# Kernel tuning notes

Measured on AMD Instinct MI355X. Metric: run time of the kernel, lower is better.

Reference implementation:

```python
import jax, jax.numpy as jnp
import numpy as np

B, S, H, DH = 2, 2048, 16, 64
D = H * DH


def setup_inputs() -> dict:
    key = jax.random.key(0)
    ks = jax.random.split(key, 10)
    std = 0.02
    return {
        "hidden_states": jax.random.normal(ks[0], (B, S, D), jnp.float32),
        "mask": jax.random.randint(ks[1], (B, S), 0, 2, jnp.int64 if jax.config.jax_enable_x64 else jnp.int32),
        "Wq": jax.random.normal(ks[2], (D, D), jnp.float32) * std,
        "bq": jnp.zeros((D,), jnp.float32),
        "Wk": jax.random.normal(ks[3], (D, D), jnp.float32) * std,
        "bk": jnp.zeros((D,), jnp.float32),
        "Wv": jax.random.normal(ks[4], (D, D), jnp.float32) * std,
        "bv": jnp.zeros((D,), jnp.float32),
        "Wo": jax.random.normal(ks[5], (D, D), jnp.float32) * std,
        "bo": jnp.zeros((D,), jnp.float32),
    }


def _split_heads(x):
    # (B, S, H*DH) -> (B, H, S, DH)
    b, s, _ = x.shape
    return x.reshape(b, s, H, DH).transpose(0, 2, 1, 3)


def reference(hidden_states, mask, Wq, bq, Wk, bk, Wv, bv, Wo, bo):
    # Linear projections (torch nn.Linear: x @ W.T + b)
    q = _split_heads(hidden_states @ Wq.T + bq)
    k = _split_heads(hidden_states @ Wk.T + bk)
    v = _split_heads(hidden_states @ Wv.T + bv)

    scale = 1.0 / np.sqrt(DH).astype(np.float32)
    scores = jnp.einsum("bhqd,bhkd->bhqk", q, k) * scale  # (B,H,S,S)
    # mask out padded key positions (mask==0 -> -inf), broadcast over heads/queries
    scores = jnp.where(mask[:, None, None, :] == 0, -jnp.inf, scores)
    weights = jax.nn.softmax(scores, axis=-1)

    attended = jnp.einsum("bhqk,bhkd->bhqd", weights, v)  # (B,H,S,DH)
    merged = attended.transpose(0, 2, 1, 3).reshape(hidden_states.shape)  # (B,S,D)
    return merged @ Wo.T + bo
```

## Files before the change

kernel.cpp:

```cpp
#include <hip/hip_runtime.h>
#include <hip/hip_bf16.h>

typedef __bf16 bf16;
typedef __bf16 bf16x4 __attribute__((ext_vector_type(4)));
typedef __bf16 bf16x8 __attribute__((ext_vector_type(8)));
typedef float f32x4 __attribute__((ext_vector_type(4)));

#define B_ 2
#define S_ 2048
#define H_ 16
#define DH_ 64
#define D_ 1024
#define NT_ 4096

#define WAIT_VMCNT0() asm volatile("s_waitcnt vmcnt(0)" ::: "memory")
#define WAIT_LGKM0()  asm volatile("s_waitcnt lgkmcnt(0)" ::: "memory")

__device__ __forceinline__ void gld_lds16(const bf16* g, bf16* l) {
    __builtin_amdgcn_global_load_lds(
        (__attribute__((address_space(1))) void*)g,
        (__attribute__((address_space(3))) void*)l, 16, 0, 0);
}

__device__ __forceinline__ bf16 f2bf(float x) {
    union { float f; unsigned u; } v; v.f = x;
    unsigned short h = (unsigned short)((v.u + 0x7FFF + ((v.u >> 16) & 1)) >> 16);
    return __builtin_bit_cast(bf16, h);
}

__global__ __launch_bounds__(256) void cvt_kernel(
    const float* __restrict__ hs,
    const float* __restrict__ Wq, const float* __restrict__ Wk,
    const float* __restrict__ Wv, const float* __restrict__ Wo,
    bf16* __restrict__ hsb, bf16* __restrict__ wqkv, bf16* __restrict__ wob)
{
    int i = (blockIdx.x * 256 + threadIdx.x) * 4;
    const float* src;
    bf16* dst;
    if (i < 4194304) {
        src = hs + i; dst = hsb + i;
    } else if (i < 7340032) {
        int off = i - 4194304;
        int which = off >> 20;
        int within = off & 1048575;
        src = (which == 0 ? Wq : which == 1 ? Wk : Wv) + within;
        dst = wqkv + off;
    } else {
        int off = i - 7340032;
        src = Wo + off; dst = wob + off;
    }
    float4 v = *(const float4*)src;
    bf16x4 o = { (bf16)v.x, (bf16)v.y, (bf16)v.z, (bf16)v.w };
    *(bf16x4*)dst = o;
}

__global__ __launch_bounds__(256, 3) void gemm_bt(
    const bf16* __restrict__ A, const bf16* __restrict__ Bm,
    const float* __restrict__ b0, const float* __restrict__ b1,
    const float* __restrict__ b2,
    bf16* __restrict__ Qo, bf16* __restrict__ Ko, bf16* __restrict__ Vt)
{
    const int K = 1024;
    __shared__ __attribute__((aligned(16))) bf16 sA[128 * 64];
    __shared__ __attribute__((aligned(16))) bf16 sB[128 * 64];

    int tid = threadIdx.x;
    int wave = tid >> 6, lane = tid & 63;
    int quad = lane >> 4, l16 = lane & 15;
    int m0 = blockIdx.x * 128;
    int n0 = blockIdx.y * 128;
    int wm = (wave & 1) * 64, wn = (wave >> 1) * 64;
    int fs = l16 & 7;

    f32x4 acc[4][4];
#pragma unroll
    for (int i = 0; i < 4; i++)
#pragma unroll
        for (int j = 0; j < 4; j++) acc[i][j] = (f32x4){0.f, 0.f, 0.f, 0.f};

    for (int k0 = 0; k0 < K; k0 += 64) {
#pragma unroll
        for (int i = 0; i < 4; i++) {
            int c = tid + i * 256;
            int row = c >> 3;
            int kc = ((c & 7) ^ (row & 7)) * 8;
            gld_lds16(A + (size_t)(m0 + row) * K + k0 + kc, &sA[c * 8]);
            gld_lds16(Bm + (size_t)(n0 + row) * K + k0 + kc, &sB[c * 8]);
        }
        WAIT_VMCNT0();
        __syncthreads();

#pragma unroll
        for (int kp = 0; kp < 2; kp++) {
            bf16x8 af[4], bfr[4];
#pragma unroll
            for (int i = 0; i < 4; i++)
                af[i] = *(const bf16x8*)&sA[(wm + i * 16 + l16) * 64 + (((kp * 4 + quad) ^ fs) * 8)];
#pragma unroll
            for (int j = 0; j < 4; j++)
                bfr[j] = *(const bf16x8*)&sB[(wn + j * 16 + l16) * 64 + (((kp * 4 + quad) ^ fs) * 8)];
#pragma unroll
            for (int i = 0; i < 4; i++)
#pragma unroll
                for (int j = 0; j < 4; j++)
                    acc[i][j] = __builtin_amdgcn_mfma_f32_16x16x32_bf16(
                        af[i], bfr[j], acc[i][j], 0, 0, 0);
        }
        __syncthreads();
    }

    const float QSCALE = 0.125f * 1.44269504088896340736f;
#pragma unroll
    for (int j = 0; j < 4; j++) {
        int n = n0 + wn + j * 16 + l16;
        int region = n >> 10;
        int nn = n & 1023;
        int h = nn >> 6, d = nn & 63;
        float bias = (region == 0 ? b0 : region == 1 ? b1 : b2)[nn];
#pragma unroll
        for (int i = 0; i < 4; i++) {
            int mb = m0 + wm + i * 16 + quad * 4;
            int b = mb >> 11, s = mb & 2047;
            int bh = b * H_ + h;
            if (region == 2) {
                bf16x4 pk = { f2bf(acc[i][j][0] + bias), f2bf(acc[i][j][1] + bias),
                              f2bf(acc[i][j][2] + bias), f2bf(acc[i][j][3] + bias) };
                *(bf16x4*)&Vt[((size_t)bh * DH_ + d) * S_ + s] = pk;
            } else {
#pragma unroll
                for (int r = 0; r < 4; r++) {
                    float v = acc[i][j][r] + bias;
                    if (region == 0)
                        Qo[((size_t)bh * S_ + s + r) * DH_ + d] = f2bf(v * QSCALE);
                    else
                        Ko[((size_t)bh * S_ + s + r) * DH_ + d] = f2bf(v);
                }
            }
        }
    }
}

__global__ __launch_bounds__(256, 2) void gemm_out(
    const bf16* __restrict__ A, const bf16* __restrict__ Bm,
    const float* __restrict__ bias0, float* __restrict__ Co)
{
    const int K = 1024;
    __shared__ __attribute__((aligned(16))) bf16 sA[128 * 64];
    __shared__ __attribute__((aligned(16))) bf16 sB[64 * 64];

    int tid = threadIdx.x;
    int wave = tid >> 6, lane = tid & 63;
    int quad = lane >> 4, l16 = lane & 15;
    int m0 = blockIdx.x * 128;
    int n0 = blockIdx.y * 64;
    int wm = (wave & 1) * 64, wn = (wave >> 1) * 32;
    int fs = l16 & 7;

    f32x4 acc[4][2];
#pragma unroll
    for (int i = 0; i < 4; i++)
#pragma unroll
        for (int j = 0; j < 2; j++) acc[i][j] = (f32x4){0.f, 0.f, 0.f, 0.f};

    for (int k0 = 0; k0 < K; k0 += 64) {
#pragma unroll
        for (int i = 0; i < 4; i++) {
            int c = tid + i * 256;
            int row = c >> 3;
            int kc = ((c & 7) ^ (row & 7)) * 8;
            gld_lds16(A + (size_t)(m0 + row) * K + k0 + kc, &sA[c * 8]);
        }
#pragma unroll
        for (int i = 0; i < 2; i++) {
            int c = tid + i * 256;
            int row = c >> 3;
            int kc = ((c & 7) ^ (row & 7)) * 8;
            gld_lds16(Bm + (size_t)(n0 + row) * K + k0 + kc, &sB[c * 8]);
        }
        WAIT_VMCNT0();
        __syncthreads();

#pragma unroll
        for (int kp = 0; kp < 2; kp++) {
            bf16x8 af[4], bfr[2];
#pragma unroll
            for (int i = 0; i < 4; i++)
                af[i] = *(const bf16x8*)&sA[(wm + i * 16 + l16) * 64 + (((kp * 4 + quad) ^ fs) * 8)];
#pragma unroll
            for (int j = 0; j < 2; j++)
                bfr[j] = *(const bf16x8*)&sB[(wn + j * 16 + l16) * 64 + (((kp * 4 + quad) ^ fs) * 8)];
#pragma unroll
            for (int i = 0; i < 4; i++)
#pragma unroll
                for (int j = 0; j < 2; j++)
                    acc[i][j] = __builtin_amdgcn_mfma_f32_16x16x32_bf16(
                        af[i], bfr[j], acc[i][j], 0, 0, 0);
        }
        __syncthreads();
    }

#pragma unroll
    for (int j = 0; j < 2; j++) {
        int n = n0 + wn + j * 16 + l16;
        float bias = bias0[n];
#pragma unroll
        for (int i = 0; i < 4; i++)
#pragma unroll
            for (int r = 0; r < 4; r++) {
                int m = m0 + wm + i * 16 + quad * 4 + r;
                Co[(size_t)m * D_ + n] = acc[i][j][r] + bias;
            }
    }
}

__global__ __launch_bounds__(256, 2) void attn_kernel(
    const bf16* __restrict__ Q, const bf16* __restrict__ Kg,
    const bf16* __restrict__ Vt, const int* __restrict__ mask,
    bf16* __restrict__ Og)
{
    __shared__ __attribute__((aligned(16))) bf16 sK[128 * 64];
    __shared__ __attribute__((aligned(16))) bf16 sV[64 * 128];
    __shared__ __attribute__((aligned(16))) bf16 sP[4][64 * 40];
    __shared__ float sMaddAll[S_];
    __shared__ float sPsumR[128];
    __shared__ float sPsumF[128];

    int tid = threadIdx.x;
    int wave = tid >> 6, lane = tid & 63;
    int quad = lane >> 4, l16 = lane & 15;
    int bh = blockIdx.y;
    int b = bh >> 4;
    int q0 = blockIdx.x * 128;
    int f8 = l16 & 7;
    int qh = wave & 1;
    int kh = wave >> 1;

    const bf16* Qb = Q + (size_t)bh * S_ * DH_;
    const bf16* Kb = Kg + (size_t)bh * S_ * DH_;
    const bf16* Vb = Vt + (size_t)bh * DH_ * S_;

#pragma unroll
    for (int i = 0; i < S_ / 256; i++) {
        int idx = tid + i * 256;
        sMaddAll[idx] = mask[b * S_ + idx] ? 0.f : -1e30f;
    }

    bf16x8 aq[4][2];
#pragma unroll
    for (int qt = 0; qt < 4; qt++) {
        int qrow = q0 + qh * 64 + qt * 16 + l16;
        aq[qt][0] = *(const bf16x8*)&Qb[(size_t)qrow * DH_ + quad * 8];
        aq[qt][1] = *(const bf16x8*)&Qb[(size_t)qrow * DH_ + 32 + quad * 8];
    }

    f32x4 o[4][4];
#pragma unroll
    for (int i = 0; i < 4; i++)
#pragma unroll
        for (int j = 0; j < 4; j++) o[i][j] = (f32x4){0.f, 0.f, 0.f, 0.f};
    float psum[4] = {0.f, 0.f, 0.f, 0.f};

    for (int kt = 0; kt < S_; kt += 128) {
#pragma unroll
        for (int i = 0; i < 8; i++) {
            int c = tid + i * 256;
            if (c < 1024) {
                int row = c >> 3;
                int g = (c & 7) ^ (row & 7);
                gld_lds16(&Kb[(size_t)(kt + row) * DH_ + g * 8], &sK[c * 8]);
            } else {
                int cv = c - 1024;
                int row = cv >> 4;
                int g = (cv & 15) ^ (row & 15);
                gld_lds16(&Vb[(size_t)row * S_ + kt + g * 8], &sV[cv * 8]);
            }
        }
        WAIT_VMCNT0();
        __syncthreads();

#pragma unroll
        for (int pass = 0; pass < 2; pass++) {
#pragma unroll
            for (int mtl = 0; mtl < 2; mtl++) {
                int keyrow = kh * 64 + pass * 32 + mtl * 16;
                bf16x8 ak0 = *(const bf16x8*)&sK[(keyrow + l16) * 64 + (quad ^ f8) * 8];
                bf16x8 ak1 = *(const bf16x8*)&sK[(keyrow + l16) * 64 + ((quad + 4) ^ f8) * 8];
                float4 ma4 = *(const float4*)&sMaddAll[kt + keyrow + quad * 4];
#pragma unroll
                for (int qt = 0; qt < 4; qt++) {
                    f32x4 c = (f32x4){0.f, 0.f, 0.f, 0.f};
                    c = __builtin_amdgcn_mfma_f32_16x16x32_bf16(ak0, aq[qt][0], c, 0, 0, 0);
                    c = __builtin_amdgcn_mfma_f32_16x16x32_bf16(ak1, aq[qt][1], c, 0, 0, 0);
                    float p0 = __builtin_amdgcn_exp2f(c[0] + ma4.x);
                    float p1 = __builtin_amdgcn_exp2f(c[1] + ma4.y);
                    float p2 = __builtin_amdgcn_exp2f(c[2] + ma4.z);
                    float p3 = __builtin_amdgcn_exp2f(c[3] + ma4.w);
                    psum[qt] += (p0 + p1) + (p2 + p3);
                    bf16x4 pk = { f2bf(p0), f2bf(p1), f2bf(p2), f2bf(p3) };
                    *(bf16x4*)&sP[wave][(qt * 16 + l16) * 40 + (mtl * 4 + quad) * 4] = pk;
                }
            }

            WAIT_LGKM0();
            bf16x8 ap[4];
#pragma unroll
            for (int qt = 0; qt < 4; qt++)
                ap[qt] = *(const bf16x8*)&sP[wave][(qt * 16 + l16) * 40 + quad * 8];
#pragma unroll
            for (int dt = 0; dt < 4; dt++) {
                int g = (kh * 8 + pass * 4 + quad) ^ l16;
                bf16x8 bv = *(const bf16x8*)&sV[(dt * 16 + l16) * 128 + g * 8];
#pragma unroll
                for (int qt = 0; qt < 4; qt++)
                    o[qt][dt] = __builtin_amdgcn_mfma_f32_16x16x32_bf16(ap[qt], bv, o[qt][dt], 0, 0, 0);
            }
        }
        __syncthreads();
    }

#pragma unroll
    for (int qt = 0; qt < 4; qt++) {
        float v = psum[qt];
        v += __shfl_xor(v, 16);
        v += __shfl_xor(v, 32);
        psum[qt] = v;
    }

    __syncthreads();
    float* sRed = (wave == 2) ? (float*)sK : (float*)sV;
    if (wave >= 2) {
#pragma unroll
        for (int qt = 0; qt < 4; qt++)
#pragma unroll
            for (int dt = 0; dt < 4; dt++)
                *(f32x4*)&sRed[((qt * 4 + dt) * 64 + lane) * 4] = o[qt][dt];
#pragma unroll
        for (int qt = 0; qt < 4; qt++)
            sPsumR[(wave - 2) * 64 + qt * 16 + l16] = psum[qt];
    }
    __syncthreads();
    if (wave < 2) {
        float* src = (wave == 0) ? (float*)sK : (float*)sV;
#pragma unroll
        for (int qt = 0; qt < 4; qt++)
#pragma unroll
            for (int dt = 0; dt < 4; dt++)
                o[qt][dt] += *(const f32x4*)&src[((qt * 4 + dt) * 64 + lane) * 4];
#pragma unroll
        for (int qt = 0; qt < 4; qt++) {
            float v = psum[qt] + sPsumR[wave * 64 + qt * 16 + l16];
            sPsumF[wave * 64 + qt * 16 + l16] = v;
        }
        WAIT_LGKM0();
        int h = bh & 15;
#pragma unroll
        for (int qt = 0; qt < 4; qt++) {
            float4 ps = *(const float4*)&sPsumF[wave * 64 + qt * 16 + quad * 4];
            float rcp[4] = { 1.f / ps.x, 1.f / ps.y, 1.f / ps.z, 1.f / ps.w };
#pragma unroll
            for (int r = 0; r < 4; r++) {
                int s = q0 + qh * 64 + qt * 16 + quad * 4 + r;
#pragma unroll
                for (int dt = 0; dt < 4; dt++) {
                    int d = dt * 16 + l16;
                    Og[((size_t)(b * S_ + s)) * D_ + h * 64 + d] = f2bf(o[qt][dt][r] * rcp[r]);
                }
            }
        }
    }
}

extern "C" void kernel_launch(void* const* d_in, const int* in_sizes, int n_in,
                              void* d_out, int out_size, void* d_ws, size_t ws_size,
                              hipStream_t stream) {
    const float* hs = (const float*)d_in[0];
    const int* mask = (const int*)d_in[1];
    const float* Wq = (const float*)d_in[2];
    const float* bq = (const float*)d_in[3];
    const float* Wk = (const float*)d_in[4];
    const float* bk = (const float*)d_in[5];
    const float* Wv = (const float*)d_in[6];
    const float* bv = (const float*)d_in[7];
    const float* Wo = (const float*)d_in[8];
    const float* bo = (const float*)d_in[9];
    float* out = (float*)d_out;

    char* ws = (char*)d_ws;
    bf16* hsb  = (bf16*)(ws);
    bf16* wqkv = (bf16*)(ws + ((size_t)8 << 20));
    bf16* wob  = (bf16*)(ws + ((size_t)14 << 20));
    bf16* Qw   = (bf16*)(ws + ((size_t)16 << 20));
    bf16* Kw   = (bf16*)(ws + ((size_t)24 << 20));
    bf16* Vtw  = (bf16*)(ws + ((size_t)32 << 20));
    bf16* attn = (bf16*)(ws + ((size_t)40 << 20));

    cvt_kernel<<<8192, 256, 0, stream>>>(hs, Wq, Wk, Wv, Wo, hsb, wqkv, wob);
    gemm_bt<<<dim3(32, 24), 256, 0, stream>>>(hsb, wqkv, bq, bk, bv,
                                              Qw, Kw, Vtw);
    attn_kernel<<<dim3(16, 32), 256, 0, stream>>>(Qw, Kw, Vtw, mask, attn);
    gemm_out<<<dim3(32, 16), 256, 0, stream>>>(attn, wob, bo, out);
}
```

Measured before the change: 197.7 us.

## Shrink attention query tile and pass P through registers via permlane swaps

The attention kernel now handles 64 query rows per block instead of 128 and launches twice as many blocks, with launch bounds raised to 4 blocks per CU. The softmax probabilities are packed with v_cvt_pk_bf16_f32 and rearranged into the MFMA A-operand layout using v_permlane32/16 swaps, which removes the per-wave sP shared-memory round trip and its wait. The mask is stored as a bf16 additive bias in LDS, halving its footprint. The aim is higher occupancy and less LDS traffic, at the cost of reloading each K/V tile for twice as many blocks.

```diff
diff --git a/kernel.cpp b/kernel.cpp
--- a/kernel.cpp
+++ b/kernel.cpp
@@ -5,13 +5,13 @@
 typedef __bf16 bf16x4 __attribute__((ext_vector_type(4)));
 typedef __bf16 bf16x8 __attribute__((ext_vector_type(8)));
 typedef float f32x4 __attribute__((ext_vector_type(4)));
+typedef unsigned short u16x4 __attribute__((ext_vector_type(4)));
 
 #define B_ 2
 #define S_ 2048
 #define H_ 16
 #define DH_ 64
 #define D_ 1024
-#define NT_ 4096
 
 #define WAIT_VMCNT0() asm volatile("s_waitcnt vmcnt(0)" ::: "memory")
 #define WAIT_LGKM0()  asm volatile("s_waitcnt lgkmcnt(0)" ::: "memory")
@@ -26,6 +26,19 @@
     union { float f; unsigned u; } v; v.f = x;
     unsigned short h = (unsigned short)((v.u + 0x7FFF + ((v.u >> 16) & 1)) >> 16);
     return __builtin_bit_cast(bf16, h);
+}
+
+__device__ __forceinline__ unsigned cvtpk(float lo, float hi) {
+    unsigned r;
+    asm("v_cvt_pk_bf16_f32 %0, %1, %2" : "=v"(r) : "v"(lo), "v"(hi));
+    return r;
+}
+
+__device__ __forceinline__ void pl32swap(unsigned &a, unsigned &b) {
+    asm("v_permlane32_swap_b32 %0, %1" : "+v"(a), "+v"(b));
+}
+__device__ __forceinline__ void pl16swap(unsigned &a, unsigned &b) {
+    asm("v_permlane16_swap_b32 %0, %1" : "+v"(a), "+v"(b));
 }
 
 __global__ __launch_bounds__(256) void cvt_kernel(
@@ -213,24 +226,23 @@
     }
 }
 
-__global__ __launch_bounds__(256, 2) void attn_kernel(
+__global__ __launch_bounds__(256, 4) void attn_kernel(
     const bf16* __restrict__ Q, const bf16* __restrict__ Kg,
     const bf16* __restrict__ Vt, const int* __restrict__ mask,
     bf16* __restrict__ Og)
 {
     __shared__ __attribute__((aligned(16))) bf16 sK[128 * 64];
     __shared__ __attribute__((aligned(16))) bf16 sV[64 * 128];
-    __shared__ __attribute__((aligned(16))) bf16 sP[4][64 * 40];
-    __shared__ float sMaddAll[S_];
-    __shared__ float sPsumR[128];
-    __shared__ float sPsumF[128];
+    __shared__ __attribute__((aligned(16))) unsigned short sMadd[S_];
+    __shared__ float sPsumR[64];
+    __shared__ float sPsumF[64];
 
     int tid = threadIdx.x;
     int wave = tid >> 6, lane = tid & 63;
     int quad = lane >> 4, l16 = lane & 15;
     int bh = blockIdx.y;
     int b = bh >> 4;
-    int q0 = blockIdx.x * 128;
+    int q0 = blockIdx.x * 64;
     int f8 = l16 & 7;
     int qh = wave & 1;
     int kh = wave >> 1;
@@ -239,26 +251,36 @@
     const bf16* Kb = Kg + (size_t)bh * S_ * DH_;
     const bf16* Vb = Vt + (size_t)bh * DH_ * S_;
 
-#pragma unroll
-    for (int i = 0; i < S_ / 256; i++) {
-        int idx = tid + i * 256;
-        sMaddAll[idx] = mask[b * S_ + idx] ? 0.f : -1e30f;
-    }
-
-    bf16x8 aq[4][2];
-#pragma unroll
-    for (int qt = 0; qt < 4; qt++) {
-        int qrow = q0 + qh * 64 + qt * 16 + l16;
+    {
+        int base = b * S_ + tid * 8;
+        int4 m0 = *(const int4*)&mask[base];
+        int4 m1 = *(const int4*)&mask[base + 4];
+        u16x4 e0 = { (unsigned short)(m0.x ? 0 : 0xF149),
+                     (unsigned short)(m0.y ? 0 : 0xF149),
+                     (unsigned short)(m0.z ? 0 : 0xF149),
+                     (unsigned short)(m0.w ? 0 : 0xF149) };
+        u16x4 e1 = { (unsigned short)(m1.x ? 0 : 0xF149),
+                     (unsigned short)(m1.y ? 0 : 0xF149),
+                     (unsigned short)(m1.z ? 0 : 0xF149),
+                     (unsigned short)(m1.w ? 0 : 0xF149) };
+        *(u16x4*)&sMadd[tid * 8] = e0;
+        *(u16x4*)&sMadd[tid * 8 + 4] = e1;
+    }
+
+    bf16x8 aq[2][2];
+#pragma unroll
+    for (int qt = 0; qt < 2; qt++) {
+        int qrow = q0 + qh * 32 + qt * 16 + l16;
         aq[qt][0] = *(const bf16x8*)&Qb[(size_t)qrow * DH_ + quad * 8];
         aq[qt][1] = *(const bf16x8*)&Qb[(size_t)qrow * DH_ + 32 + quad * 8];
     }
 
-    f32x4 o[4][4];
-#pragma unroll
-    for (int i = 0; i < 4; i++)
+    f32x4 o[2][4];
+#pragma unroll
+    for (int i = 0; i < 2; i++)
 #pragma unroll
         for (int j = 0; j < 4; j++) o[i][j] = (f32x4){0.f, 0.f, 0.f, 0.f};
-    float psum[4] = {0.f, 0.f, 0.f, 0.f};
+    float psum[2] = {0.f, 0.f};
 
     for (int kt = 0; kt < S_; kt += 128) {
 #pragma unroll
@@ -280,38 +302,50 @@
 
 #pragma unroll
         for (int pass = 0; pass < 2; pass++) {
+            unsigned w01[2][2], w23[2][2];
 #pragma unroll
             for (int mtl = 0; mtl < 2; mtl++) {
                 int keyrow = kh * 64 + pass * 32 + mtl * 16;
-                bf16x8 ak0 = *(const bf16x8*)&sK[(keyrow + l16) * 64 + (quad ^ f8) * 8];
-                bf16x8 ak1 = *(const bf16x8*)&sK[(keyrow + l16) * 64 + ((quad + 4) ^ f8) * 8];
-                float4 ma4 = *(const float4*)&sMaddAll[kt + keyrow + quad * 4];
-#pragma unroll
-                for (int qt = 0; qt < 4; qt++) {
+                bf16x8 ak0 = *(const bf16x8*)&sK[(keyrow + l16) * 64 + ((quad ^ f8) * 8)];
+                bf16x8 ak1 = *(const bf16x8*)&sK[(keyrow + l16) * 64 + (((quad + 4) ^ f8) * 8)];
+                u16x4 mm = *(const u16x4*)&sMadd[kt + keyrow + quad * 4];
+                float ma0 = __builtin_bit_cast(float, (unsigned)mm.x << 16);
+                float ma1 = __builtin_bit_cast(float, (unsigned)mm.y << 16);
+                float ma2 = __builtin_bit_cast(float, (unsigned)mm.z << 16);
+                float ma3 = __builtin_bit_cast(float, (unsigned)mm.w << 16);
+#pragma unroll
+                for (int qt = 0; qt < 2; qt++) {
                     f32x4 c = (f32x4){0.f, 0.f, 0.f, 0.f};
                     c = __builtin_amdgcn_mfma_f32_16x16x32_bf16(ak0, aq[qt][0], c, 0, 0, 0);
                     c = __builtin_amdgcn_mfma_f32_16x16x32_bf16(ak1, aq[qt][1], c, 0, 0, 0);
-                    float p0 = __builtin_amdgcn_exp2f(c[0] + ma4.x);
-                    float p1 = __builtin_amdgcn_exp2f(c[1] + ma4.y);
-                    float p2 = __builtin_amdgcn_exp2f(c[2] + ma4.z);
-                    float p3 = __builtin_amdgcn_exp2f(c[3] + ma4.w);
+                    float p0 = __builtin_amdgcn_exp2f(c[0] + ma0);
+                    float p1 = __builtin_amdgcn_exp2f(c[1] + ma1);
+                    float p2 = __builtin_amdgcn_exp2f(c[2] + ma2);
+                    float p3 = __builtin_amdgcn_exp2f(c[3] + ma3);
                     psum[qt] += (p0 + p1) + (p2 + p3);
-                    bf16x4 pk = { f2bf(p0), f2bf(p1), f2bf(p2), f2bf(p3) };
-                    *(bf16x4*)&sP[wave][(qt * 16 + l16) * 40 + (mtl * 4 + quad) * 4] = pk;
+                    w01[qt][mtl] = cvtpk(p0, p1);
+                    w23[qt][mtl] = cvtpk(p2, p3);
                 }
             }
 
-            WAIT_LGKM0();
-            bf16x8 ap[4];
-#pragma unroll
-            for (int qt = 0; qt < 4; qt++)
-                ap[qt] = *(const bf16x8*)&sP[wave][(qt * 16 + l16) * 40 + quad * 8];
+            bf16x8 ap[2];
+#pragma unroll
+            for (int qt = 0; qt < 2; qt++) {
+                unsigned r0 = w01[qt][0], r2 = w01[qt][1];
+                pl32swap(r0, r2); pl16swap(r0, r2);
+                unsigned r1 = w23[qt][0], r3 = w23[qt][1];
+                pl32swap(r1, r3); pl16swap(r1, r3);
+                union { unsigned u[4]; bf16x8 v; } U;
+                U.u[0] = r0; U.u[1] = r1; U.u[2] = r2; U.u[3] = r3;
+                ap[qt] = U.v;
+            }
+
 #pragma unroll
             for (int dt = 0; dt < 4; dt++) {
                 int g = (kh * 8 + pass * 4 + quad) ^ l16;
                 bf16x8 bv = *(const bf16x8*)&sV[(dt * 16 + l16) * 128 + g * 8];
 #pragma unroll
-                for (int qt = 0; qt < 4; qt++)
+                for (int qt = 0; qt < 2; qt++)
                     o[qt][dt] = __builtin_amdgcn_mfma_f32_16x16x32_bf16(ap[qt], bv, o[qt][dt], 0, 0, 0);
             }
         }
@@ -319,7 +353,7 @@
     }
 
 #pragma unroll
-    for (int qt = 0; qt < 4; qt++) {
+    for (int qt = 0; qt < 2; qt++) {
         float v = psum[qt];
         v += __shfl_xor(v, 16);
         v += __shfl_xor(v, 32);
@@ -330,36 +364,34 @@
     float* sRed = (wave == 2) ? (float*)sK : (float*)sV;
     if (wave >= 2) {
 #pragma unroll
-        for (int qt = 0; qt < 4; qt++)
+        for (int qt = 0; qt < 2; qt++)
 #pragma unroll
             for (int dt = 0; dt < 4; dt++)
                 *(f32x4*)&sRed[((qt * 4 + dt) * 64 + lane) * 4] = o[qt][dt];
 #pragma unroll
-        for (int qt = 0; qt < 4; qt++)
-            sPsumR[(wave - 2) * 64 + qt * 16 + l16] = psum[qt];
+        for (int qt = 0; qt < 2; qt++)
+            sPsumR[(wave - 2) * 32 + qt * 16 + l16] = psum[qt];
     }
     __syncthreads();
     if (wave < 2) {
         float* src = (wave == 0) ? (float*)sK : (float*)sV;
 #pragma unroll
-        for (int qt = 0; qt < 4; qt++)
+        for (int qt = 0; qt < 2; qt++)
 #pragma unroll
             for (int dt = 0; dt < 4; dt++)
                 o[qt][dt] += *(const f32x4*)&src[((qt * 4 + dt) * 64 + lane) * 4];
 #pragma unroll
-        for (int qt = 0; qt < 4; qt++) {
-            float v = psum[qt] + sPsumR[wave * 64 + qt * 16 + l16];
-            sPsumF[wave * 64 + qt * 16 + l16] = v;
-        }
+        for (int qt = 0; qt < 2; qt++)
+            sPsumF[wave * 32 + qt * 16 + l16] = psum[qt] + sPsumR[wave * 32 + qt * 16 + l16];
         WAIT_LGKM0();
         int h = bh & 15;
 #pragma unroll
-        for (int qt = 0; qt < 4; qt++) {
-            float4 ps = *(const float4*)&sPsumF[wave * 64 + qt * 16 + quad * 4];
+        for (int qt = 0; qt < 2; qt++) {
+            float4 ps = *(const float4*)&sPsumF[wave * 32 + qt * 16 + quad * 4];
             float rcp[4] = { 1.f / ps.x, 1.f / ps.y, 1.f / ps.z, 1.f / ps.w };
 #pragma unroll
             for (int r = 0; r < 4; r++) {
-                int s = q0 + qh * 64 + qt * 16 + quad * 4 + r;
+                int s = q0 + wave * 32 + qt * 16 + quad * 4 + r;
 #pragma unroll
                 for (int dt = 0; dt < 4; dt++) {
                     int d = dt * 16 + l16;
@@ -397,6 +429,6 @@
     cvt_kernel<<<8192, 256, 0, stream>>>(hs, Wq, Wk, Wv, Wo, hsb, wqkv, wob);
     gemm_bt<<<dim3(32, 24), 256, 0, stream>>>(hsb, wqkv, bq, bk, bv,
                                               Qw, Kw, Vtw);
-    attn_kernel<<<dim3(16, 32), 256, 0, stream>>>(Qw, Kw, Vtw, mask, attn);
+    attn_kernel<<<dim3(32, 32), 256, 0, stream>>>(Qw, Kw, Vtw, mask, attn);
     gemm_out<<<dim3(32, 16), 256, 0, stream>>>(attn, wob, bo, out);
 }
```

Result: faster. 189.2 us (-4.3%).
